# Kernel optimization log

Measured on AMD Instinct MI355X. Metric: run time of the kernel, lower is better.

Reference implementation:

```python
import jax, jax.numpy as jnp
import numpy as np

N_NODES = 50000
N_EDGES = 800000
IN_DIM = 100
OUT_DIM = 40
K_HOPS = 3


def setup_inputs() -> dict:
    key = jax.random.key(0)
    k1, k2, k3, k4 = jax.random.split(key, 4)
    feat = jax.random.normal(k1, (N_NODES, IN_DIM), dtype=jnp.float32)
    # fc params (PyTorch Linear default init scale ~ 1/sqrt(in_dim))
    W = jax.random.normal(k2, (OUT_DIM, IN_DIM), dtype=jnp.float32) / np.sqrt(IN_DIM)
    b = jnp.zeros((OUT_DIM,), dtype=jnp.float32)
    src = jax.random.randint(k3, (N_EDGES,), 0, N_NODES, dtype=jnp.int32)
    dst = jax.random.randint(k4, (N_EDGES,), 0, N_NODES, dtype=jnp.int32)
    return {"feat": feat, "W": W, "b": b, "src": src, "dst": dst}


def reference(feat, W, b, src, dst):
    n = feat.shape[0]
    # symmetric degree norm (DGL SGConv uses in-degrees, clamp(min=1))
    deg = jax.ops.segment_sum(jnp.ones_like(dst, dtype=feat.dtype), dst, num_segments=n)
    norm = jnp.maximum(deg, 1.0)[:, None] ** -0.5  # [N,1]
    h = feat
    for _ in range(K_HOPS):
        h = h * norm
        # SpMM: sum over incoming edges (gather src rows, scatter-add to dst)
        h = jax.ops.segment_sum(h[src], dst, num_segments=n)
        h = h * norm
    # user-supplied normalize: per-feature zero mean / unit std (unbiased std)
    h = (h - h.mean(axis=0)) / h.std(axis=0, ddof=1)
    # final linear classifier
    return h @ W.T + b
```

## Files before the change

### kernel.cpp

```cpp
#include <hip/hip_runtime.h>

#define N_NODES 50000
#define N_EDGES 800000
#define IN_DIM 100
#define OUT_DIM 40
#define ROW 50
#define ROW_PAD 64
#define SCAN_B 512
#define NSCAN_BLK ((N_NODES + SCAN_B - 1) / SCAN_B)
#define CSR_CAP (N_EDGES + N_NODES * 8 + 64)

typedef unsigned int uint;

__device__ __forceinline__ float bflo(uint u) { return __uint_as_float(u << 16); }
__device__ __forceinline__ float bfhi(uint u) { return __uint_as_float(u & 0xffff0000u); }
__device__ __forceinline__ uint packbf(float a, float b) {
    uint ua = __float_as_uint(a), ub = __float_as_uint(b);
    ua = (ua + 0x7fffu + ((ua >> 16) & 1u)) >> 16;
    ub = (ub + 0x7fffu + ((ub >> 16) & 1u)) >> 16;
    return ua | (ub << 16);
}

__global__ void deg_kernel(const int* __restrict__ dst, int* __restrict__ deg,
                           int* __restrict__ eoff) {
    int e = blockIdx.x * blockDim.x + threadIdx.x;
    if (e < N_EDGES) eoff[e] = atomicAdd(&deg[dst[e]], 1);
}

__global__ __launch_bounds__(SCAN_B) void scan1_kernel(const int* __restrict__ deg,
                                                       int* __restrict__ rowptr,
                                                       float* __restrict__ norm,
                                                       float* __restrict__ norm2,
                                                       int* __restrict__ blocksum) {
    int i = blockIdx.x * SCAN_B + threadIdx.x;
    int lane = threadIdx.x & 63, wid = threadIdx.x >> 6;
    int d = (i < N_NODES) ? deg[i] : 0;
    int da = (d + 7) & ~7;
    int v = da;
#pragma unroll
    for (int off = 1; off < 64; off <<= 1) {
        int t = __shfl_up(v, off);
        if (lane >= off) v += t;
    }
    __shared__ int wsum[8];
    if (lane == 63) wsum[wid] = v;
    __syncthreads();
    if (threadIdx.x < 8) {
        int w = wsum[threadIdx.x];
#pragma unroll
        for (int off = 1; off < 8; off <<= 1) {
            int t = __shfl_up(w, off);
            if (lane >= off) w += t;
        }
        wsum[threadIdx.x] = w;
    }
    __syncthreads();
    int woff = wid ? wsum[wid - 1] : 0;
    int incl = woff + v;
    if (i < N_NODES) {
        rowptr[i] = incl - da;
        float n1 = 1.0f / sqrtf((float)max(d, 1));
        norm[i] = n1;
        norm2[i] = n1 * n1;
    }
    if (threadIdx.x == SCAN_B - 1) blocksum[blockIdx.x] = incl;
}

__global__ __launch_bounds__(SCAN_B) void scan23_kernel(int* __restrict__ rowptr,
                                                        const int* __restrict__ blocksum,
                                                        const int* __restrict__ deg,
                                                        int* __restrict__ csr) {
    __shared__ int s_boff, s_tot;
    int t = threadIdx.x, bb = blockIdx.x;
    if (t == 0) {
        int boff = 0, tot = 0;
        for (int j = 0; j < NSCAN_BLK; ++j) {
            int v = blocksum[j];
            tot += v;
            if (j < bb) boff += v;
        }
        s_boff = boff;
        s_tot = tot;
    }
    __syncthreads();
    int i = bb * SCAN_B + t;
    if (i < N_NODES) {
        int rp = rowptr[i] + s_boff;
        rowptr[i] = rp;
        int d = deg[i], da = (d + 7) & ~7;
        for (int k = d; k < da; ++k) csr[rp + k] = N_NODES;
    }
    if (bb == 0 && t == 0) rowptr[N_NODES] = s_tot;
}

__global__ __launch_bounds__(256) void fill_kernel(const int* __restrict__ src,
                                                   const int* __restrict__ dst,
                                                   const int* __restrict__ rowptr,
                                                   const int* __restrict__ eoff,
                                                   int* __restrict__ csr,
                                                   const float* __restrict__ feat,
                                                   const float* __restrict__ norm,
                                                   uint4* __restrict__ fs4,
                                                   uint4* __restrict__ bufA4,
                                                   uint4* __restrict__ bufB4) {
    const int T1 = N_EDGES, T2 = N_NODES * 16;
    int task = blockIdx.x * 256 + threadIdx.x;
    if (task < T1) {
        csr[rowptr[dst[task]] + eoff[task]] = src[task];
    } else if (task < T1 + T2) {
        int qq = task - T1;
        int n = qq >> 4, ql = qq & 15;
        float nm = norm[n];
        uint4 o = make_uint4(0u, 0u, 0u, 0u);
        const float4* fr = (const float4*)(feat + (size_t)n * IN_DIM);
        if (ql < 12) {
            float4 a = fr[2 * ql], b2 = fr[2 * ql + 1];
            o.x = packbf(a.x * nm, a.y * nm);  o.y = packbf(a.z * nm, a.w * nm);
            o.z = packbf(b2.x * nm, b2.y * nm); o.w = packbf(b2.z * nm, b2.w * nm);
        } else if (ql == 12) {
            float4 a = fr[24];
            o.x = packbf(a.x * nm, a.y * nm);  o.y = packbf(a.z * nm, a.w * nm);
        }
        fs4[qq] = o;
    } else if (task < T1 + T2 + 48) {
        int k = task - T1 - T2;
        uint4 z = make_uint4(0u, 0u, 0u, 0u);
        uint4* dp = (k < 16) ? fs4 : (k < 32) ? bufA4 : bufB4;
        dp[(size_t)N_NODES * 16 + (k & 15)] = z;
    }
}

__global__ __launch_bounds__(128) void spmm_kernel(const uint4* __restrict__ H4,
                                                   const int* __restrict__ rowptr,
                                                   const int* __restrict__ csr,
                                                   const float* __restrict__ scale,
                                                   uint4* __restrict__ out4) {
    const int n = blockIdx.x * 2 + (threadIdx.x >> 6);
    const int l = threadIdx.x & 63;
    const int q = l >> 4;
    const int ql = l & 15;
    const int beg = rowptr[n], end = rowptr[n + 1];
    float ax0 = 0.f, ax1 = 0.f, ax2 = 0.f, ax3 = 0.f;
    float ay0 = 0.f, ay1 = 0.f, ay2 = 0.f, ay3 = 0.f;
#pragma unroll 2
    for (int j = beg; j < end; j += 8) {
        int s0 = csr[j + q];
        int s1 = csr[j + 4 + q];
        uint4 u0 = H4[(size_t)s0 * 16 + ql];
        uint4 u1 = H4[(size_t)s1 * 16 + ql];
        ax0 += bflo(u0.x); ay0 += bfhi(u0.x);
        ax1 += bflo(u0.y); ay1 += bfhi(u0.y);
        ax2 += bflo(u0.z); ay2 += bfhi(u0.z);
        ax3 += bflo(u0.w); ay3 += bfhi(u0.w);
        ax0 += bflo(u1.x); ay0 += bfhi(u1.x);
        ax1 += bflo(u1.y); ay1 += bfhi(u1.y);
        ax2 += bflo(u1.z); ay2 += bfhi(u1.z);
        ax3 += bflo(u1.w); ay3 += bfhi(u1.w);
    }
    ax0 += __shfl_xor(ax0, 16); ax1 += __shfl_xor(ax1, 16);
    ax2 += __shfl_xor(ax2, 16); ax3 += __shfl_xor(ax3, 16);
    ay0 += __shfl_xor(ay0, 16); ay1 += __shfl_xor(ay1, 16);
    ay2 += __shfl_xor(ay2, 16); ay3 += __shfl_xor(ay3, 16);
    ax0 += __shfl_xor(ax0, 32); ax1 += __shfl_xor(ax1, 32);
    ax2 += __shfl_xor(ax2, 32); ax3 += __shfl_xor(ax3, 32);
    ay0 += __shfl_xor(ay0, 32); ay1 += __shfl_xor(ay1, 32);
    ay2 += __shfl_xor(ay2, 32); ay3 += __shfl_xor(ay3, 32);
    if (q == 0) {
        float sc = scale[n];
        uint4 o;
        o.x = packbf(ax0 * sc, ay0 * sc);
        o.y = packbf(ax1 * sc, ay1 * sc);
        o.z = packbf(ax2 * sc, ay2 * sc);
        o.w = packbf(ax3 * sc, ay3 * sc);
        out4[(size_t)n * 16 + ql] = o;
    }
}

#define CS_BLOCKS 625
#define CS_THREADS 256
__global__ __launch_bounds__(CS_THREADS) void col_stats_kernel(const uint* __restrict__ h,
                                                               float* __restrict__ colsum,
                                                               float* __restrict__ colsq) {
    int gtid = blockIdx.x * CS_THREADS + threadIdx.x;
    const int stride = CS_BLOCKS * CS_THREADS;
    const int total = N_NODES * ROW_PAD;
    float s0 = 0.f, s1 = 0.f, q0 = 0.f, q1 = 0.f;
    for (int i = gtid; i < total; i += stride) {
        uint u = h[i];
        float a = bflo(u), b = bfhi(u);
        s0 += a; s1 += b; q0 += a * a; q1 += b * b;
    }
    __shared__ float ssum[IN_DIM], ssq[IN_DIM];
    if (threadIdx.x < IN_DIM) { ssum[threadIdx.x] = 0.f; ssq[threadIdx.x] = 0.f; }
    __syncthreads();
    int p = gtid & 63;
    if (p < ROW) {
        atomicAdd(&ssum[2 * p], s0);
        atomicAdd(&ssum[2 * p + 1], s1);
        atomicAdd(&ssq[2 * p], q0);
        atomicAdd(&ssq[2 * p + 1], q1);
    }
    __syncthreads();
    if (threadIdx.x < IN_DIM) {
        atomicAdd(&colsum[threadIdx.x], ssum[threadIdx.x]);
        atomicAdd(&colsq[threadIdx.x], ssq[threadIdx.x]);
    }
}

__global__ __launch_bounds__(256) void final_kernel(const uint4* __restrict__ h4,
                                                    const float* __restrict__ colsum,
                                                    const float* __restrict__ colsq,
                                                    const float* __restrict__ W,
                                                    const float* __restrict__ b,
                                                    float* __restrict__ out) {
    __shared__ float sW[104 * OUT_DIM];
    __shared__ float sb[OUT_DIM];
    const float Nf = (float)N_NODES;
    for (int i = threadIdx.x; i < 104 * OUT_DIM; i += 256) {
        int f = i / OUT_DIM, o = i - f * OUT_DIM;
        float wv = 0.f;
        if (f < IN_DIM) {
            float m = colsum[f] / Nf;
            float var = fmaxf((colsq[f] - Nf * m * m) / (Nf - 1.0f), 1e-20f);
            wv = W[o * IN_DIM + f] * rsqrtf(var);
        }
        sW[i] = wv;
    }
    if (threadIdx.x < OUT_DIM) {
        float acc = b[threadIdx.x];
        for (int f = 0; f < IN_DIM; ++f) {
            float m = colsum[f] / Nf;
            float var = fmaxf((colsq[f] - Nf * m * m) / (Nf - 1.0f), 1e-20f);
            acc -= m * W[threadIdx.x * IN_DIM + f] * rsqrtf(var);
        }
        sb[threadIdx.x] = acc;
    }
    __syncthreads();
    int t = blockIdx.x * 256 + threadIdx.x;
    if (t >= N_NODES * 10) return;
    int n = t / 10;
    int og = (t - n * 10) * 4;
    const uint4* hr = h4 + (size_t)n * 16;
    float a0 = sb[og], a1 = sb[og + 1], a2 = sb[og + 2], a3 = sb[og + 3];
#pragma unroll
    for (int r = 0; r < 13; ++r) {
        uint4 u = hr[r];
        int f = r * 8;
        float v0 = bflo(u.x), v1 = bfhi(u.x), v2 = bflo(u.y), v3 = bfhi(u.y);
        float v4 = bflo(u.z), v5 = bfhi(u.z), v6 = bflo(u.w), v7 = bfhi(u.w);
        const float* w0 = &sW[(f + 0) * OUT_DIM + og];
        const float* w1 = &sW[(f + 1) * OUT_DIM + og];
        const float* w2 = &sW[(f + 2) * OUT_DIM + og];
        const float* w3 = &sW[(f + 3) * OUT_DIM + og];
        const float* w4 = &sW[(f + 4) * OUT_DIM + og];
        const float* w5 = &sW[(f + 5) * OUT_DIM + og];
        const float* w6 = &sW[(f + 6) * OUT_DIM + og];
        const float* w7 = &sW[(f + 7) * OUT_DIM + og];
        a0 += v0 * w0[0] + v1 * w1[0] + v2 * w2[0] + v3 * w3[0]
            + v4 * w4[0] + v5 * w5[0] + v6 * w6[0] + v7 * w7[0];
        a1 += v0 * w0[1] + v1 * w1[1] + v2 * w2[1] + v3 * w3[1]
            + v4 * w4[1] + v5 * w5[1] + v6 * w6[1] + v7 * w7[1];
        a2 += v0 * w0[2] + v1 * w1[2] + v2 * w2[2] + v3 * w3[2]
            + v4 * w4[2] + v5 * w5[2] + v6 * w6[2] + v7 * w7[2];
        a3 += v0 * w0[3] + v1 * w1[3] + v2 * w2[3] + v3 * w3[3]
            + v4 * w4[3] + v5 * w5[3] + v6 * w6[3] + v7 * w7[3];
    }
    float4 o = make_float4(a0, a1, a2, a3);
    *((float4*)(out + (size_t)n * OUT_DIM + og)) = o;
}

extern "C" void kernel_launch(void* const* d_in, const int* in_sizes, int n_in,
                              void* d_out, int out_size, void* d_ws, size_t ws_size,
                              hipStream_t stream) {
    const float* feat = (const float*)d_in[0];
    const float* W    = (const float*)d_in[1];
    const float* b    = (const float*)d_in[2];
    const int*   src  = (const int*)d_in[3];
    const int*   dst  = (const int*)d_in[4];
    float* out = (float*)d_out;

    char* w = (char*)d_ws;
    int*   deg      = (int*)w;    w += N_NODES * 4;
    float* colsum   = (float*)w;  w += 128 * 4;
    float* colsq    = (float*)w;  w += 128 * 4;
    int*   eoff     = (int*)w;    w += N_EDGES * 4;
    int*   rowptr   = (int*)w;    w += 50004 * 4;
    float* norm     = (float*)w;  w += N_NODES * 4;
    float* norm2    = (float*)w;  w += N_NODES * 4;
    int*   blocksum = (int*)w;    w += 128 * 4;
    int*   csr      = (int*)w;    w += CSR_CAP * 4;
    w = (char*)(((size_t)w + 255) & ~(size_t)255);
    const size_t HB = (size_t)(N_NODES + 1) * ROW_PAD * 4;
    uint*  fs       = (uint*)w;   w += HB;
    uint*  bufA     = (uint*)w;   w += HB;
    uint*  bufB     = (uint*)w;   w += HB;

    hipMemsetAsync(d_ws, 0, (size_t)(N_NODES + 256) * 4, stream);
    deg_kernel<<<(N_EDGES + 255) / 256, 256, 0, stream>>>(dst, deg, eoff);
    scan1_kernel<<<NSCAN_BLK, SCAN_B, 0, stream>>>(deg, rowptr, norm, norm2, blocksum);
    scan23_kernel<<<NSCAN_BLK, SCAN_B, 0, stream>>>(rowptr, blocksum, deg, csr);
    {
        int total = N_EDGES + N_NODES * 16 + 48;
        fill_kernel<<<(total + 255) / 256, 256, 0, stream>>>(
            src, dst, rowptr, eoff, csr, feat, norm,
            (uint4*)fs, (uint4*)bufA, (uint4*)bufB);
    }
    spmm_kernel<<<N_NODES / 2, 128, 0, stream>>>((const uint4*)fs, rowptr, csr, norm2, (uint4*)bufA);
    spmm_kernel<<<N_NODES / 2, 128, 0, stream>>>((const uint4*)bufA, rowptr, csr, norm2, (uint4*)bufB);
    spmm_kernel<<<N_NODES / 2, 128, 0, stream>>>((const uint4*)bufB, rowptr, csr, norm, (uint4*)bufA);
    col_stats_kernel<<<CS_BLOCKS, CS_THREADS, 0, stream>>>(bufA, colsum, colsq);
    {
        int total = N_NODES * 10;
        final_kernel<<<(total + 255) / 256, 256, 0, stream>>>(
            (const uint4*)bufA, colsum, colsq, W, b, out);
    }
}
```

Measured before the change: 270.8 us.

## Switch intermediate features from bf16 to fp16 with packed half2 accumulation

Feature rows are stored as fp16 instead of bf16, and the SpMM accumulates with packed __hadd2 in half precision instead of unpacking to fp32. The edge loop now consumes 4 edges per step with one gather per lane, so CSR row padding shrinks from multiples of 8 to multiples of 4. Together these are meant to cut ALU unpack work, register use and padded gather traffic in the memory-bound SpMM. The cost is lower accumulation precision and overflow risk for high-degree nodes, since sums stay in fp16 through the cross-lane reduction.

```diff
diff --git a/kernel.cpp b/kernel.cpp
--- a/kernel.cpp
+++ b/kernel.cpp
@@ -1,4 +1,5 @@
 #include <hip/hip_runtime.h>
+#include <hip/hip_fp16.h>
 
 #define N_NODES 50000
 #define N_EDGES 800000
@@ -8,17 +9,16 @@
 #define ROW_PAD 64
 #define SCAN_B 512
 #define NSCAN_BLK ((N_NODES + SCAN_B - 1) / SCAN_B)
-#define CSR_CAP (N_EDGES + N_NODES * 8 + 64)
+#define CSR_CAP (N_EDGES + N_NODES * 4 + 64)
 
 typedef unsigned int uint;
 
-__device__ __forceinline__ float bflo(uint u) { return __uint_as_float(u << 16); }
-__device__ __forceinline__ float bfhi(uint u) { return __uint_as_float(u & 0xffff0000u); }
-__device__ __forceinline__ uint packbf(float a, float b) {
-    uint ua = __float_as_uint(a), ub = __float_as_uint(b);
-    ua = (ua + 0x7fffu + ((ua >> 16) & 1u)) >> 16;
-    ub = (ub + 0x7fffu + ((ub >> 16) & 1u)) >> 16;
-    return ua | (ub << 16);
+__device__ __forceinline__ __half2 u2h(uint u) { union { uint u; __half2 h; } c; c.u = u; return c.h; }
+__device__ __forceinline__ uint h2u(__half2 h) { union { uint u; __half2 h; } c; c.h = h; return c.u; }
+__device__ __forceinline__ __half2 h2shfl_xor(__half2 v, int m) {
+    float f = __uint_as_float(h2u(v));
+    f = __shfl_xor(f, m);
+    return u2h(__float_as_uint(f));
 }
 
 __global__ void deg_kernel(const int* __restrict__ dst, int* __restrict__ deg,
@@ -35,7 +35,7 @@
     int i = blockIdx.x * SCAN_B + threadIdx.x;
     int lane = threadIdx.x & 63, wid = threadIdx.x >> 6;
     int d = (i < N_NODES) ? deg[i] : 0;
-    int da = (d + 7) & ~7;
+    int da = (d + 3) & ~3;
     int v = da;
 #pragma unroll
     for (int off = 1; off < 64; off <<= 1) {
@@ -87,7 +87,7 @@
     if (i < N_NODES) {
         int rp = rowptr[i] + s_boff;
         rowptr[i] = rp;
-        int d = deg[i], da = (d + 7) & ~7;
+        int d = deg[i], da = (d + 3) & ~3;
         for (int k = d; k < da; ++k) csr[rp + k] = N_NODES;
     }
     if (bb == 0 && t == 0) rowptr[N_NODES] = s_tot;
@@ -115,11 +115,14 @@
         const float4* fr = (const float4*)(feat + (size_t)n * IN_DIM);
         if (ql < 12) {
             float4 a = fr[2 * ql], b2 = fr[2 * ql + 1];
-            o.x = packbf(a.x * nm, a.y * nm);  o.y = packbf(a.z * nm, a.w * nm);
-            o.z = packbf(b2.x * nm, b2.y * nm); o.w = packbf(b2.z * nm, b2.w * nm);
+            o.x = h2u(__floats2half2_rn(a.x * nm, a.y * nm));
+            o.y = h2u(__floats2half2_rn(a.z * nm, a.w * nm));
+            o.z = h2u(__floats2half2_rn(b2.x * nm, b2.y * nm));
+            o.w = h2u(__floats2half2_rn(b2.z * nm, b2.w * nm));
         } else if (ql == 12) {
             float4 a = fr[24];
-            o.x = packbf(a.x * nm, a.y * nm);  o.y = packbf(a.z * nm, a.w * nm);
+            o.x = h2u(__floats2half2_rn(a.x * nm, a.y * nm));
+            o.y = h2u(__floats2half2_rn(a.z * nm, a.w * nm));
         }
         fs4[qq] = o;
     } else if (task < T1 + T2 + 48) {
@@ -140,38 +143,33 @@
     const int q = l >> 4;
     const int ql = l & 15;
     const int beg = rowptr[n], end = rowptr[n + 1];
-    float ax0 = 0.f, ax1 = 0.f, ax2 = 0.f, ax3 = 0.f;
-    float ay0 = 0.f, ay1 = 0.f, ay2 = 0.f, ay3 = 0.f;
-#pragma unroll 2
-    for (int j = beg; j < end; j += 8) {
-        int s0 = csr[j + q];
-        int s1 = csr[j + 4 + q];
-        uint4 u0 = H4[(size_t)s0 * 16 + ql];
-        uint4 u1 = H4[(size_t)s1 * 16 + ql];
-        ax0 += bflo(u0.x); ay0 += bfhi(u0.x);
-        ax1 += bflo(u0.y); ay1 += bfhi(u0.y);
-        ax2 += bflo(u0.z); ay2 += bfhi(u0.z);
-        ax3 += bflo(u0.w); ay3 += bfhi(u0.w);
-        ax0 += bflo(u1.x); ay0 += bfhi(u1.x);
-        ax1 += bflo(u1.y); ay1 += bfhi(u1.y);
-        ax2 += bflo(u1.z); ay2 += bfhi(u1.z);
-        ax3 += bflo(u1.w); ay3 += bfhi(u1.w);
-    }
-    ax0 += __shfl_xor(ax0, 16); ax1 += __shfl_xor(ax1, 16);
-    ax2 += __shfl_xor(ax2, 16); ax3 += __shfl_xor(ax3, 16);
-    ay0 += __shfl_xor(ay0, 16); ay1 += __shfl_xor(ay1, 16);
-    ay2 += __shfl_xor(ay2, 16); ay3 += __shfl_xor(ay3, 16);
-    ax0 += __shfl_xor(ax0, 32); ax1 += __shfl_xor(ax1, 32);
-    ax2 += __shfl_xor(ax2, 32); ax3 += __shfl_xor(ax3, 32);
-    ay0 += __shfl_xor(ay0, 32); ay1 += __shfl_xor(ay1, 32);
-    ay2 += __shfl_xor(ay2, 32); ay3 += __shfl_xor(ay3, 32);
+    __half2 a0 = u2h(0u), a1 = u2h(0u), a2 = u2h(0u), a3 = u2h(0u);
+#pragma unroll 4
+    for (int j = beg; j < end; j += 4) {
+        int s = csr[j + q];
+        uint4 u = H4[(size_t)s * 16 + ql];
+        a0 = __hadd2(a0, u2h(u.x));
+        a1 = __hadd2(a1, u2h(u.y));
+        a2 = __hadd2(a2, u2h(u.z));
+        a3 = __hadd2(a3, u2h(u.w));
+    }
+    a0 = __hadd2(a0, h2shfl_xor(a0, 16));
+    a1 = __hadd2(a1, h2shfl_xor(a1, 16));
+    a2 = __hadd2(a2, h2shfl_xor(a2, 16));
+    a3 = __hadd2(a3, h2shfl_xor(a3, 16));
+    a0 = __hadd2(a0, h2shfl_xor(a0, 32));
+    a1 = __hadd2(a1, h2shfl_xor(a1, 32));
+    a2 = __hadd2(a2, h2shfl_xor(a2, 32));
+    a3 = __hadd2(a3, h2shfl_xor(a3, 32));
     if (q == 0) {
         float sc = scale[n];
+        float2 f0 = __half22float2(a0), f1 = __half22float2(a1);
+        float2 f2 = __half22float2(a2), f3 = __half22float2(a3);
         uint4 o;
-        o.x = packbf(ax0 * sc, ay0 * sc);
-        o.y = packbf(ax1 * sc, ay1 * sc);
-        o.z = packbf(ax2 * sc, ay2 * sc);
-        o.w = packbf(ax3 * sc, ay3 * sc);
+        o.x = h2u(__floats2half2_rn(f0.x * sc, f0.y * sc));
+        o.y = h2u(__floats2half2_rn(f1.x * sc, f1.y * sc));
+        o.z = h2u(__floats2half2_rn(f2.x * sc, f2.y * sc));
+        o.w = h2u(__floats2half2_rn(f3.x * sc, f3.y * sc));
         out4[(size_t)n * 16 + ql] = o;
     }
 }
@@ -186,9 +184,8 @@
     const int total = N_NODES * ROW_PAD;
     float s0 = 0.f, s1 = 0.f, q0 = 0.f, q1 = 0.f;
     for (int i = gtid; i < total; i += stride) {
-        uint u = h[i];
-        float a = bflo(u), b = bfhi(u);
-        s0 += a; s1 += b; q0 += a * a; q1 += b * b;
+        float2 f = __half22float2(u2h(h[i]));
+        s0 += f.x; s1 += f.y; q0 += f.x * f.x; q1 += f.y * f.y;
     }
     __shared__ float ssum[IN_DIM], ssq[IN_DIM];
     if (threadIdx.x < IN_DIM) { ssum[threadIdx.x] = 0.f; ssq[threadIdx.x] = 0.f; }
@@ -246,8 +243,10 @@
     for (int r = 0; r < 13; ++r) {
         uint4 u = hr[r];
         int f = r * 8;
-        float v0 = bflo(u.x), v1 = bfhi(u.x), v2 = bflo(u.y), v3 = bfhi(u.y);
-        float v4 = bflo(u.z), v5 = bfhi(u.z), v6 = bflo(u.w), v7 = bfhi(u.w);
+        float2 p0 = __half22float2(u2h(u.x)), p1 = __half22float2(u2h(u.y));
+        float2 p2 = __half22float2(u2h(u.z)), p3 = __half22float2(u2h(u.w));
+        float v0 = p0.x, v1 = p0.y, v2 = p1.x, v3 = p1.y;
+        float v4 = p2.x, v5 = p2.y, v6 = p3.x, v7 = p3.y;
         const float* w0 = &sW[(f + 0) * OUT_DIM + og];
         const float* w1 = &sW[(f + 1) * OUT_DIM + og];
         const float* w2 = &sW[(f + 2) * OUT_DIM + og];
```

Result: no change. 269.6 us (-0.5%).
